# Performance work log

Measured on AMD Instinct MI355X. Metric: run time of the kernel, lower is better.

Reference implementation:

```python
import jax, jax.numpy as jnp
import numpy as np

N_NODES = 100000
EPS = 1e-12  # torch F.normalize eps


def setup_inputs() -> dict:
    key = jax.random.key(0)
    ks = jax.random.split(key, 8)
    F_IN, H, C, E = 128, 128, 8, 1600000
    s = 1.0 / np.sqrt(F_IN)
    return {
        "x": jax.random.normal(ks[0], (N_NODES, F_IN), dtype=jnp.float32),
        "edge_index": jax.random.randint(ks[1], (2, E), 0, N_NODES, dtype=jnp.int64),
        "W1": jax.random.normal(ks[2], (F_IN, H), dtype=jnp.float32) * s,
        "b1": jnp.zeros((H,), jnp.float32),
        "W2": jax.random.normal(ks[3], (H, H), dtype=jnp.float32) * s,
        "b2": jnp.zeros((H,), jnp.float32),
        "W3": jax.random.normal(ks[4], (H, H), dtype=jnp.float32) * s,
        "b3": jnp.zeros((H,), jnp.float32),
        "Wlin": jax.random.normal(ks[5], (3 * H, C), dtype=jnp.float32) * (1.0 / np.sqrt(3 * H)),
        "blin": jnp.zeros((C,), jnp.float32),
    }


def _gcn_norm(edge_index, n):
    # add self-loops, compute symmetric D^-1/2 A D^-1/2 edge weights
    loops = jnp.arange(n, dtype=edge_index.dtype)
    src = jnp.concatenate([edge_index[0], loops])
    dst = jnp.concatenate([edge_index[1], loops])
    deg = jax.ops.segment_sum(jnp.ones_like(dst, dtype=jnp.float32), dst, num_segments=n)
    dinv = jnp.where(deg > 0, jax.lax.rsqrt(deg), 0.0)
    norm = dinv[src] * dinv[dst]  # [E + N]
    return src, dst, norm


def _gcn_layer(x, W, b, src, dst, norm, n):
    h = x @ W                              # dense transform [N, H]
    msg = h[src] * norm[:, None]           # gather + scale  [E+N, H]
    agg = jax.ops.segment_sum(msg, dst, num_segments=n)  # scatter-add [N, H]
    h = jax.nn.relu(agg + b)
    nrm = jnp.sqrt(jnp.sum(h * h, axis=1, keepdims=True))
    return h / jnp.maximum(nrm, EPS)       # L2-normalize per node


def reference(x, edge_index, W1, b1, W2, b2, W3, b3, Wlin, blin):
    n = x.shape[0]
    src, dst, norm = _gcn_norm(edge_index, n)
    out1 = _gcn_layer(x, W1, b1, src, dst, norm, n)
    out2 = _gcn_layer(out1, W2, b2, src, dst, norm, n)
    out3 = _gcn_layer(out2, W3, b3, src, dst, norm, n)
    emb = jnp.concatenate([out1, out2, out3], axis=1)  # [N, 3H]
    logits = emb @ Wlin + blin
    return jax.nn.log_softmax(logits, axis=1)
```

## Files before the change

kernel.cpp:

```cpp
#include <hip/hip_runtime.h>
#include <math.h>


__device__ __forceinline__ int edge_val(const int* e32, int is64, long long idx) {
  return is64 ? e32[idx * 2] : e32[idx];
}

__device__ __forceinline__ unsigned short f2bf(float f) {
  unsigned int u = __float_as_uint(f);
  u += 0x7fff + ((u >> 16) & 1);
  return (unsigned short)(u >> 16);
}

__device__ __forceinline__ float2 bfpair(unsigned int u) {
  return make_float2(__uint_as_float(u << 16), __uint_as_float(u & 0xffff0000u));
}

__global__ void prep_k(const int* e32, int* flag, int* counts, int* cursor, int n) {
  int stride = gridDim.x * blockDim.x;
  for (int j = blockIdx.x * blockDim.x + threadIdx.x; j < n; j += stride) {
    counts[j] = 0; cursor[j] = 0;
  }
  if (blockIdx.x == 0) {
    __shared__ int any;
    if (threadIdx.x == 0) any = 0;
    __syncthreads();
    int v = 0;
    for (int k = threadIdx.x; k < 4096; k += blockDim.x) v |= e32[2 * k + 1];
    if (v) atomicOr(&any, 1);
    __syncthreads();
    if (threadIdx.x == 0) *flag = (any == 0) ? 1 : 0;
  }
}

__global__ void count_k(const int* e32, const int* flag, int* counts, int E) {
  int is64 = *flag;
  long long i = (long long)blockIdx.x * blockDim.x + threadIdx.x;
  long long stride = (long long)gridDim.x * blockDim.x;
  for (; i < E; i += stride) {
    int d = edge_val(e32, is64, (long long)E + i);
    atomicAdd(&counts[d], 1);
  }
}

__global__ __launch_bounds__(1024) void scan1_k(const int* counts, int* partials,
                                                float* dinv, int n) {
  __shared__ int sb[1024];
  int i = blockIdx.x * 1024 + threadIdx.x;
  int v = (i < n) ? counts[i] : 0;
  if (i < n) dinv[i] = 1.0f / sqrtf((float)v + 1.0f);
  sb[threadIdx.x] = v;
  __syncthreads();
  for (int off = 512; off > 0; off >>= 1) {
    if (threadIdx.x < off) sb[threadIdx.x] += sb[threadIdx.x + off];
    __syncthreads();
  }
  if (threadIdx.x == 0) partials[blockIdx.x] = sb[0];
}

__global__ void scan2_k(int* partials, int nb) {
  if (blockIdx.x == 0 && threadIdx.x == 0) {
    int run = 0;
    for (int i = 0; i < nb; i++) { int v = partials[i]; partials[i] = run; run += v; }
  }
}

__global__ __launch_bounds__(1024) void scan3_k(const int* counts, const int* partials,
                                                int* row_ptr, int n) {
  __shared__ int sb[1024];
  int i = blockIdx.x * 1024 + threadIdx.x;
  int v = (i < n) ? counts[i] : 0;
  sb[threadIdx.x] = v;
  __syncthreads();
  for (int off = 1; off < 1024; off <<= 1) {
    int add = (threadIdx.x >= (unsigned)off) ? sb[threadIdx.x - off] : 0;
    __syncthreads();
    sb[threadIdx.x] += add;
    __syncthreads();
  }
  if (i < n) row_ptr[i] = partials[blockIdx.x] + sb[threadIdx.x] - v;
}

__global__ void fill_k(const int* e32, const int* flag, const int* row_ptr, int* cursor,
                       const float* dinv, int2* edata, int E) {
  int is64 = *flag;
  long long i = (long long)blockIdx.x * blockDim.x + threadIdx.x;
  long long stride = (long long)gridDim.x * blockDim.x;
  for (; i < E; i += stride) {
    int s = edge_val(e32, is64, i);
    int d = edge_val(e32, is64, (long long)E + i);
    int pos = atomicAdd(&cursor[d], 1);
    int idx = row_ptr[d] + pos;
    edata[idx] = make_int2(s, __float_as_int(dinv[s] * dinv[d]));
  }
}

__global__ __launch_bounds__(256) void dense_k(const float* __restrict__ X,
                                               const float* __restrict__ W,
                                               unsigned short* __restrict__ Hout, int n) {
  __shared__ float Wl[128 * 128];
  for (int i = threadIdx.x; i < 4096; i += 256)
    ((float4*)Wl)[i] = ((const float4*)W)[i];
  __syncthreads();
  int cg = threadIdx.x & 31;
  int rg = threadIdx.x >> 5;
  int row0 = blockIdx.x * 64 + rg * 8;
  float4 acc[8];
#pragma unroll
  for (int r = 0; r < 8; r++) acc[r] = make_float4(0.f, 0.f, 0.f, 0.f);
  const float4* Wl4 = (const float4*)Wl;
  for (int k4 = 0; k4 < 32; k4++) {
    float4 w0 = Wl4[(k4 * 4 + 0) * 32 + cg];
    float4 w1 = Wl4[(k4 * 4 + 1) * 32 + cg];
    float4 w2 = Wl4[(k4 * 4 + 2) * 32 + cg];
    float4 w3 = Wl4[(k4 * 4 + 3) * 32 + cg];
#pragma unroll
    for (int r = 0; r < 8; r++) {
      int row = row0 + r; if (row >= n) row = n - 1;
      float4 xv = *(const float4*)(X + (size_t)row * 128 + k4 * 4);
      acc[r].x += xv.x * w0.x + xv.y * w1.x + xv.z * w2.x + xv.w * w3.x;
      acc[r].y += xv.x * w0.y + xv.y * w1.y + xv.z * w2.y + xv.w * w3.y;
      acc[r].z += xv.x * w0.z + xv.y * w1.z + xv.z * w2.z + xv.w * w3.z;
      acc[r].w += xv.x * w0.w + xv.y * w1.w + xv.z * w2.w + xv.w * w3.w;
    }
  }
#pragma unroll
  for (int r = 0; r < 8; r++) {
    int row = row0 + r;
    if (row < n) {
      unsigned int u0 = (unsigned int)f2bf(acc[r].x) | ((unsigned int)f2bf(acc[r].y) << 16);
      unsigned int u1 = (unsigned int)f2bf(acc[r].z) | ((unsigned int)f2bf(acc[r].w) << 16);
      *(uint2*)&Hout[(size_t)row * 128 + cg * 4] = make_uint2(u0, u1);
    }
  }
}

__global__ __launch_bounds__(256) void agg_k(const unsigned short* __restrict__ H,
                                             const int2* __restrict__ edata,
                                             const int* __restrict__ row_ptr,
                                             const int* __restrict__ counts,
                                             const float* __restrict__ dinv,
                                             const float* __restrict__ bias,
                                             float* __restrict__ Out, int n) {
  int node = blockIdx.x * 4 + (threadIdx.x >> 6);
  if (node >= n) return;
  int lane = threadIdx.x & 63;
  float di = dinv[node];
  float wself = di * di;
  unsigned int us = *(const unsigned int*)(H + (size_t)node * 128 + lane * 2);
  float2 hs = bfpair(us);
  float ax = hs.x * wself, ay = hs.y * wself;
  int start = row_ptr[node];
  int cnt = counts[node];
  for (int base = 0; base < cnt; base += 64) {
    int m = min(64, cnt - base);
    int2 me = (lane < m) ? edata[start + base + lane] : make_int2(0, 0);
    int i = 0;
    for (; i + 4 <= m; i += 4) {
      int s0 = __shfl(me.x, i),     s1 = __shfl(me.x, i + 1);
      int s2 = __shfl(me.x, i + 2), s3 = __shfl(me.x, i + 3);
      float w0 = __int_as_float(__shfl(me.y, i));
      float w1 = __int_as_float(__shfl(me.y, i + 1));
      float w2 = __int_as_float(__shfl(me.y, i + 2));
      float w3 = __int_as_float(__shfl(me.y, i + 3));
      unsigned int u0 = *(const unsigned int*)(H + (size_t)s0 * 128 + lane * 2);
      unsigned int u1 = *(const unsigned int*)(H + (size_t)s1 * 128 + lane * 2);
      unsigned int u2 = *(const unsigned int*)(H + (size_t)s2 * 128 + lane * 2);
      unsigned int u3 = *(const unsigned int*)(H + (size_t)s3 * 128 + lane * 2);
      float2 f0 = bfpair(u0), f1 = bfpair(u1), f2 = bfpair(u2), f3 = bfpair(u3);
      ax += f0.x * w0 + f1.x * w1 + f2.x * w2 + f3.x * w3;
      ay += f0.y * w0 + f1.y * w1 + f2.y * w2 + f3.y * w3;
    }
    for (; i < m; i++) {
      int s0 = __shfl(me.x, i);
      float w0 = __int_as_float(__shfl(me.y, i));
      unsigned int u0 = *(const unsigned int*)(H + (size_t)s0 * 128 + lane * 2);
      float2 f0 = bfpair(u0);
      ax += f0.x * w0;
      ay += f0.y * w0;
    }
  }
  float2 bv = *(const float2*)&bias[lane * 2];
  ax = fmaxf(ax + bv.x, 0.f);
  ay = fmaxf(ay + bv.y, 0.f);
  float ss = ax * ax + ay * ay;
#pragma unroll
  for (int off = 32; off > 0; off >>= 1) ss += __shfl_xor(ss, off);
  float scale = 1.0f / fmaxf(sqrtf(ss), 1e-12f);
  *(float2*)&Out[(size_t)node * 128 + lane * 2] = make_float2(ax * scale, ay * scale);
}

__global__ __launch_bounds__(256) void final_k(const float* __restrict__ O1,
                                               const float* __restrict__ O2,
                                               const float* __restrict__ O3,
                                               const float* __restrict__ Wlin,
                                               const float* __restrict__ blin,
                                               float* __restrict__ out, int n) {
  __shared__ float Wl[384 * 8];
  __shared__ float bl[8];
  for (int i = threadIdx.x; i < 384 * 8 / 4; i += 256)
    ((float4*)Wl)[i] = ((const float4*)Wlin)[i];
  if (threadIdx.x < 8) bl[threadIdx.x] = blin[threadIdx.x];
  __syncthreads();
  int node = blockIdx.x * 256 + threadIdx.x;
  if (node >= n) return;
  float acc[8];
#pragma unroll
  for (int c = 0; c < 8; c++) acc[c] = bl[c];
  const float* parts[3] = {O1, O2, O3};
  for (int p = 0; p < 3; p++) {
    const float4* e4 = (const float4*)(parts[p] + (size_t)node * 128);
    for (int k4 = 0; k4 < 32; k4++) {
      float4 v = e4[k4];
      const float4* wr = (const float4*)&Wl[(p * 128 + k4 * 4) * 8];
      float vv[4] = {v.x, v.y, v.z, v.w};
#pragma unroll
      for (int j = 0; j < 4; j++) {
        float4 wa = wr[j * 2], wb = wr[j * 2 + 1];
        acc[0] += vv[j] * wa.x; acc[1] += vv[j] * wa.y;
        acc[2] += vv[j] * wa.z; acc[3] += vv[j] * wa.w;
        acc[4] += vv[j] * wb.x; acc[5] += vv[j] * wb.y;
        acc[6] += vv[j] * wb.z; acc[7] += vv[j] * wb.w;
      }
    }
  }
  float mx = acc[0];
#pragma unroll
  for (int c = 1; c < 8; c++) mx = fmaxf(mx, acc[c]);
  float se = 0.f;
#pragma unroll
  for (int c = 0; c < 8; c++) se += expf(acc[c] - mx);
  float lse = mx + logf(se);
  float* o = out + (size_t)node * 8;
#pragma unroll
  for (int c = 0; c < 8; c++) o[c] = acc[c] - lse;
}

extern "C" void kernel_launch(void* const* d_in, const int* in_sizes, int n_in,
                              void* d_out, int out_size, void* d_ws, size_t ws_size,
                              hipStream_t stream) {
  const float* x    = (const float*)d_in[0];
  const int*   e32  = (const int*)d_in[1];
  const float* W1   = (const float*)d_in[2];
  const float* b1   = (const float*)d_in[3];
  const float* W2   = (const float*)d_in[4];
  const float* b2   = (const float*)d_in[5];
  const float* W3   = (const float*)d_in[6];
  const float* b3   = (const float*)d_in[7];
  const float* Wlin = (const float*)d_in[8];
  const float* blin = (const float*)d_in[9];
  float* out = (float*)d_out;

  const int Nn = in_sizes[0] / 128;
  const int E  = in_sizes[1] / 2;

  char* ws = (char*)d_ws;
  size_t off = 0;
  auto take = [&](size_t bytes) -> char* {
    char* p = ws + off;
    off = (off + bytes + 255) & ~(size_t)255;
    return p;
  };
  int*   flag   = (int*)  take(256);
  int*   counts = (int*)  take((size_t)Nn * 4);
  int*   cursor = (int*)  take((size_t)Nn * 4);
  int*   rowp   = (int*)  take((size_t)Nn * 4);
  float* dinv   = (float*)take((size_t)Nn * 4);
  int*   parts  = (int*)  take(4096);
  int2*  edata  = (int2*) take((size_t)E * 8);
  unsigned short* Hb = (unsigned short*)take((size_t)Nn * 128 * 2);
  float* O1     = (float*)take((size_t)Nn * 128 * 4);
  float* O2     = (float*)take((size_t)Nn * 128 * 4);
  float* O3     = (float*)take((size_t)Nn * 128 * 4);

  int nb = (Nn + 1023) / 1024;
  int dense_grid = (Nn + 63) / 64;
  int agg_grid = (Nn + 3) / 4;

  hipLaunchKernelGGL(prep_k,  dim3(256),  dim3(256),  0, stream, e32, flag, counts, cursor, Nn);
  hipLaunchKernelGGL(count_k, dim3(2048), dim3(256),  0, stream, e32, flag, counts, E);
  hipLaunchKernelGGL(scan1_k, dim3(nb),   dim3(1024), 0, stream, counts, parts, dinv, Nn);
  hipLaunchKernelGGL(scan2_k, dim3(1),    dim3(1),    0, stream, parts, nb);
  hipLaunchKernelGGL(scan3_k, dim3(nb),   dim3(1024), 0, stream, counts, parts, rowp, Nn);
  hipLaunchKernelGGL(fill_k,  dim3(2048), dim3(256),  0, stream, e32, flag, rowp, cursor, dinv, edata, E);

  hipLaunchKernelGGL(dense_k, dim3(dense_grid), dim3(256), 0, stream, x,  W1, Hb, Nn);
  hipLaunchKernelGGL(agg_k,   dim3(agg_grid),   dim3(256), 0, stream, Hb, edata, rowp, counts, dinv, b1, O1, Nn);
  hipLaunchKernelGGL(dense_k, dim3(dense_grid), dim3(256), 0, stream, O1, W2, Hb, Nn);
  hipLaunchKernelGGL(agg_k,   dim3(agg_grid),   dim3(256), 0, stream, Hb, edata, rowp, counts, dinv, b2, O2, Nn);
  hipLaunchKernelGGL(dense_k, dim3(dense_grid), dim3(256), 0, stream, O2, W3, Hb, Nn);
  hipLaunchKernelGGL(agg_k,   dim3(agg_grid),   dim3(256), 0, stream, Hb, edata, rowp, counts, dinv, b3, O3, Nn);
  hipLaunchKernelGGL(final_k, dim3((Nn + 255) / 256), dim3(256), 0, stream, O1, O2, O3, Wlin, blin, out, Nn);
}
```

Baseline: 743.8 us.

## Use bf16 MFMA for dense transforms and store layer outputs in bf16

Replaces the fp32 FMA dense kernel with a bf16 MFMA 16x16x32 kernel. Inputs and weights are converted to bf16 first, with the weights transposed. Layer outputs O1-O3 are now stored as bf16 instead of fp32, which halves the traffic for the next dense step and for the final classifier. The cost is lower precision in the intermediate embeddings and the dense inputs, plus extra conversion launches and scattered 2-byte output stores.

Result: faster. 605.8 us (-18.5%).

```diff
diff --git a/kernel.cpp b/kernel.cpp
--- a/kernel.cpp
+++ b/kernel.cpp
@@ -1,6 +1,9 @@
 #include <hip/hip_runtime.h>
 #include <math.h>
 
+
+typedef __attribute__((ext_vector_type(8))) short short8;
+typedef __attribute__((ext_vector_type(4))) float float4v;
 
 __device__ __forceinline__ int edge_val(const int* e32, int is64, long long idx) {
   return is64 ? e32[idx * 2] : e32[idx];
@@ -10,6 +13,10 @@
   unsigned int u = __float_as_uint(f);
   u += 0x7fff + ((u >> 16) & 1);
   return (unsigned short)(u >> 16);
+}
+
+__device__ __forceinline__ float bf2f(unsigned short h) {
+  return __uint_as_float((unsigned int)h << 16);
 }
 
 __device__ __forceinline__ float2 bfpair(unsigned int u) {
@@ -95,42 +102,53 @@
   }
 }
 
-__global__ __launch_bounds__(256) void dense_k(const float* __restrict__ X,
-                                               const float* __restrict__ W,
-                                               unsigned short* __restrict__ Hout, int n) {
-  __shared__ float Wl[128 * 128];
-  for (int i = threadIdx.x; i < 4096; i += 256)
-    ((float4*)Wl)[i] = ((const float4*)W)[i];
-  __syncthreads();
-  int cg = threadIdx.x & 31;
-  int rg = threadIdx.x >> 5;
-  int row0 = blockIdx.x * 64 + rg * 8;
-  float4 acc[8];
-#pragma unroll
-  for (int r = 0; r < 8; r++) acc[r] = make_float4(0.f, 0.f, 0.f, 0.f);
-  const float4* Wl4 = (const float4*)Wl;
-  for (int k4 = 0; k4 < 32; k4++) {
-    float4 w0 = Wl4[(k4 * 4 + 0) * 32 + cg];
-    float4 w1 = Wl4[(k4 * 4 + 1) * 32 + cg];
-    float4 w2 = Wl4[(k4 * 4 + 2) * 32 + cg];
-    float4 w3 = Wl4[(k4 * 4 + 3) * 32 + cg];
-#pragma unroll
-    for (int r = 0; r < 8; r++) {
-      int row = row0 + r; if (row >= n) row = n - 1;
-      float4 xv = *(const float4*)(X + (size_t)row * 128 + k4 * 4);
-      acc[r].x += xv.x * w0.x + xv.y * w1.x + xv.z * w2.x + xv.w * w3.x;
-      acc[r].y += xv.x * w0.y + xv.y * w1.y + xv.z * w2.y + xv.w * w3.y;
-      acc[r].z += xv.x * w0.z + xv.y * w1.z + xv.z * w2.z + xv.w * w3.z;
-      acc[r].w += xv.x * w0.w + xv.y * w1.w + xv.z * w2.w + xv.w * w3.w;
-    }
-  }
-#pragma unroll
-  for (int r = 0; r < 8; r++) {
-    int row = row0 + r;
-    if (row < n) {
-      unsigned int u0 = (unsigned int)f2bf(acc[r].x) | ((unsigned int)f2bf(acc[r].y) << 16);
-      unsigned int u1 = (unsigned int)f2bf(acc[r].z) | ((unsigned int)f2bf(acc[r].w) << 16);
-      *(uint2*)&Hout[(size_t)row * 128 + cg * 4] = make_uint2(u0, u1);
+__global__ void wconv_k(const float* __restrict__ W, unsigned short* __restrict__ Wt) {
+  int t = blockIdx.x * blockDim.x + threadIdx.x;
+  if (t >= 128 * 128) return;
+  int col = t >> 7, k = t & 127;
+  Wt[t] = f2bf(W[k * 128 + col]);
+}
+
+__global__ void xconv_k(const float* __restrict__ x, unsigned short* __restrict__ xb,
+                        int total4) {
+  int i = blockIdx.x * blockDim.x + threadIdx.x;
+  int stride = gridDim.x * blockDim.x;
+  for (; i < total4; i += stride) {
+    float4 v = ((const float4*)x)[i];
+    unsigned int u0 = (unsigned int)f2bf(v.x) | ((unsigned int)f2bf(v.y) << 16);
+    unsigned int u1 = (unsigned int)f2bf(v.z) | ((unsigned int)f2bf(v.w) << 16);
+    ((uint2*)xb)[i] = make_uint2(u0, u1);
+  }
+}
+
+__global__ __launch_bounds__(256) void dense_mfma_k(
+    const unsigned short* __restrict__ Xb, const unsigned short* __restrict__ Wt,
+    unsigned short* __restrict__ Hout, int n) {
+  int wave = threadIdx.x >> 6;
+  int lane = threadIdx.x & 63;
+  int row0 = blockIdx.x * 64 + wave * 16;
+  int lm = lane & 15;
+  int lk = lane >> 4;
+  int arow = row0 + lm; if (arow >= n) arow = n - 1;
+  const unsigned short* xp = Xb + (size_t)arow * 128 + lk * 8;
+  short8 a[4];
+#pragma unroll
+  for (int kk = 0; kk < 4; kk++)
+    a[kk] = *reinterpret_cast<const short8*>(xp + kk * 32);
+#pragma unroll
+  for (int nt = 0; nt < 8; nt++) {
+    float4v acc = {0.f, 0.f, 0.f, 0.f};
+    const unsigned short* wp = Wt + (size_t)(nt * 16 + lm) * 128 + lk * 8;
+#pragma unroll
+    for (int kk = 0; kk < 4; kk++) {
+      short8 b = *reinterpret_cast<const short8*>(wp + kk * 32);
+      acc = __builtin_amdgcn_mfma_f32_16x16x32_bf16(a[kk], b, acc, 0, 0, 0);
+    }
+    int col = nt * 16 + lm;
+#pragma unroll
+    for (int r = 0; r < 4; r++) {
+      int row = row0 + lk * 4 + r;
+      if (row < n) Hout[(size_t)row * 128 + col] = f2bf(acc[r]);
     }
   }
 }
@@ -141,7 +159,7 @@
                                              const int* __restrict__ counts,
                                              const float* __restrict__ dinv,
                                              const float* __restrict__ bias,
-                                             float* __restrict__ Out, int n) {
+                                             unsigned short* __restrict__ Out, int n) {
   int node = blockIdx.x * 4 + (threadIdx.x >> 6);
   if (node >= n) return;
   int lane = threadIdx.x & 63;
@@ -174,8 +192,7 @@
     for (; i < m; i++) {
       int s0 = __shfl(me.x, i);
       float w0 = __int_as_float(__shfl(me.y, i));
-      unsigned int u0 = *(const unsigned int*)(H + (size_t)s0 * 128 + lane * 2);
-      float2 f0 = bfpair(u0);
+      float2 f0 = bfpair(*(const unsigned int*)(H + (size_t)s0 * 128 + lane * 2));
       ax += f0.x * w0;
       ay += f0.y * w0;
     }
@@ -187,12 +204,13 @@
 #pragma unroll
   for (int off = 32; off > 0; off >>= 1) ss += __shfl_xor(ss, off);
   float scale = 1.0f / fmaxf(sqrtf(ss), 1e-12f);
-  *(float2*)&Out[(size_t)node * 128 + lane * 2] = make_float2(ax * scale, ay * scale);
-}
-
-__global__ __launch_bounds__(256) void final_k(const float* __restrict__ O1,
-                                               const float* __restrict__ O2,
-                                               const float* __restrict__ O3,
+  unsigned int po = (unsigned int)f2bf(ax * scale) | ((unsigned int)f2bf(ay * scale) << 16);
+  *(unsigned int*)(Out + (size_t)node * 128 + lane * 2) = po;
+}
+
+__global__ __launch_bounds__(256) void final_k(const unsigned short* __restrict__ O1,
+                                               const unsigned short* __restrict__ O2,
+                                               const unsigned short* __restrict__ O3,
                                                const float* __restrict__ Wlin,
                                                const float* __restrict__ blin,
                                                float* __restrict__ out, int n) {
@@ -207,13 +225,14 @@
   float acc[8];
 #pragma unroll
   for (int c = 0; c < 8; c++) acc[c] = bl[c];
-  const float* parts[3] = {O1, O2, O3};
+  const unsigned short* parts[3] = {O1, O2, O3};
   for (int p = 0; p < 3; p++) {
-    const float4* e4 = (const float4*)(parts[p] + (size_t)node * 128);
+    const uint2* e2 = (const uint2*)(parts[p] + (size_t)node * 128);
     for (int k4 = 0; k4 < 32; k4++) {
-      float4 v = e4[k4];
+      uint2 v = e2[k4];
+      float2 fa = bfpair(v.x), fb = bfpair(v.y);
+      float vv[4] = {fa.x, fa.y, fb.x, fb.y};
       const float4* wr = (const float4*)&Wl[(p * 128 + k4 * 4) * 8];
-      float vv[4] = {v.x, v.y, v.z, v.w};
 #pragma unroll
       for (int j = 0; j < 4; j++) {
         float4 wa = wr[j * 2], wb = wr[j * 2 + 1];
@@ -268,10 +287,14 @@
   float* dinv   = (float*)take((size_t)Nn * 4);
   int*   parts  = (int*)  take(4096);
   int2*  edata  = (int2*) take((size_t)E * 8);
-  unsigned short* Hb = (unsigned short*)take((size_t)Nn * 128 * 2);
-  float* O1     = (float*)take((size_t)Nn * 128 * 4);
-  float* O2     = (float*)take((size_t)Nn * 128 * 4);
-  float* O3     = (float*)take((size_t)Nn * 128 * 4);
+  unsigned short* xb  = (unsigned short*)take((size_t)Nn * 128 * 2);
+  unsigned short* Hb  = (unsigned short*)take((size_t)Nn * 128 * 2);
+  unsigned short* O1  = (unsigned short*)take((size_t)Nn * 128 * 2);
+  unsigned short* O2  = (unsigned short*)take((size_t)Nn * 128 * 2);
+  unsigned short* O3  = (unsigned short*)take((size_t)Nn * 128 * 2);
+  unsigned short* Wt1 = (unsigned short*)take(128 * 128 * 2);
+  unsigned short* Wt2 = (unsigned short*)take(128 * 128 * 2);
+  unsigned short* Wt3 = (unsigned short*)take(128 * 128 * 2);
 
   int nb = (Nn + 1023) / 1024;
   int dense_grid = (Nn + 63) / 64;
@@ -284,11 +307,16 @@
   hipLaunchKernelGGL(scan3_k, dim3(nb),   dim3(1024), 0, stream, counts, parts, rowp, Nn);
   hipLaunchKernelGGL(fill_k,  dim3(2048), dim3(256),  0, stream, e32, flag, rowp, cursor, dinv, edata, E);
 
-  hipLaunchKernelGGL(dense_k, dim3(dense_grid), dim3(256), 0, stream, x,  W1, Hb, Nn);
-  hipLaunchKernelGGL(agg_k,   dim3(agg_grid),   dim3(256), 0, stream, Hb, edata, rowp, counts, dinv, b1, O1, Nn);
-  hipLaunchKernelGGL(dense_k, dim3(dense_grid), dim3(256), 0, stream, O1, W2, Hb, Nn);
-  hipLaunchKernelGGL(agg_k,   dim3(agg_grid),   dim3(256), 0, stream, Hb, edata, rowp, counts, dinv, b2, O2, Nn);
-  hipLaunchKernelGGL(dense_k, dim3(dense_grid), dim3(256), 0, stream, O2, W3, Hb, Nn);
-  hipLaunchKernelGGL(agg_k,   dim3(agg_grid),   dim3(256), 0, stream, Hb, edata, rowp, counts, dinv, b3, O3, Nn);
+  hipLaunchKernelGGL(wconv_k, dim3(64), dim3(256), 0, stream, W1, Wt1);
+  hipLaunchKernelGGL(wconv_k, dim3(64), dim3(256), 0, stream, W2, Wt2);
+  hipLaunchKernelGGL(wconv_k, dim3(64), dim3(256), 0, stream, W3, Wt3);
+  hipLaunchKernelGGL(xconv_k, dim3(2048), dim3(256), 0, stream, x, xb, Nn * 32);
+
+  hipLaunchKernelGGL(dense_mfma_k, dim3(dense_grid), dim3(256), 0, stream, xb, Wt1, Hb, Nn);
+  hipLaunchKernelGGL(agg_k,        dim3(agg_grid),   dim3(256), 0, stream, Hb, edata, rowp, counts, dinv, b1, O1, Nn);
+  hipLaunchKernelGGL(dense_mfma_k, dim3(dense_grid), dim3(256), 0, stream, O1, Wt2, Hb, Nn);
+  hipLaunchKernelGGL(agg_k,        dim3(agg_grid),   dim3(256), 0, stream, Hb, edata, rowp, counts, dinv, b2, O2, Nn);
+  hipLaunchKernelGGL(dense_mfma_k, dim3(dense_grid), dim3(256), 0, stream, O2, Wt3, Hb, Nn);
+  hipLaunchKernelGGL(agg_k,        dim3(agg_grid),   dim3(256), 0, stream, Hb, edata, rowp, counts, dinv, b3, O3, Nn);
   hipLaunchKernelGGL(final_k, dim3((Nn + 255) / 256), dim3(256), 0, stream, O1, O2, O3, Wlin, blin, out, Nn);
 }
```
